# Optimization experiments

Hardware: AMD Instinct MI355X
Metric: run time of the kernel (lower is better)

## Reference

```python
import jax, jax.numpy as jnp
import numpy as np

NU, NI, E = 200000, 100000, 500000
D, H, O = 128, 256, 128  # embedding_dim, hidden_dim, output_dim


def _sage(x_src, x_dst, src, dst, n_dst, W_l, b_l, W_r):
    """PyG SAGEConv (mean aggr): lin_l(mean_j x_src[j]) + lin_r(x_dst)."""
    msgs = x_src[src]                                            # [E, d_in]
    summed = jax.ops.segment_sum(msgs, dst, num_segments=n_dst)  # [n_dst, d_in]
    deg = jax.ops.segment_sum(jnp.ones(src.shape, x_src.dtype), dst, num_segments=n_dst)
    mean = summed / jnp.maximum(deg, 1.0)[:, None]
    return mean @ W_l + b_l + x_dst @ W_r


def setup_inputs() -> dict:
    key = jax.random.key(0)
    ks = jax.random.split(key, 18)

    def w(k, i, o):
        return jax.random.normal(k, (i, o), jnp.float32) / np.float32(np.sqrt(i))

    return {
        "x_user": jax.random.normal(ks[0], (NU, D), jnp.float32),
        "x_item": jax.random.normal(ks[1], (NI, D), jnp.float32),
        "edge_src": jax.random.randint(ks[2], (E,), 0, NU, jnp.int32),
        "edge_dst": jax.random.randint(ks[3], (E,), 0, NI, jnp.int32),
        # layer 1 (encoder): D -> H, one SAGEConv per edge type
        "W_l1_ui": w(ks[4], D, H), "W_r1_ui": w(ks[5], D, H), "b_l1_ui": jnp.zeros((H,), jnp.float32),
        "W_l1_iu": w(ks[6], D, H), "W_r1_iu": w(ks[7], D, H), "b_l1_iu": jnp.zeros((H,), jnp.float32),
        # layer 2 (projection): H -> O
        "W_l2_ui": w(ks[8], H, O), "W_r2_ui": w(ks[9], H, O), "b_l2_ui": jnp.zeros((O,), jnp.float32),
        "W_l2_iu": w(ks[10], H, O), "W_r2_iu": w(ks[11], H, O), "b_l2_iu": jnp.zeros((O,), jnp.float32),
    }


def reference(x_user, x_item, edge_src, edge_dst,
              W_l1_ui, W_r1_ui, b_l1_ui, W_l1_iu, W_r1_iu, b_l1_iu,
              W_l2_ui, W_r2_ui, b_l2_ui, W_l2_iu, W_r2_iu, b_l2_iu):
    # encoder layer: relu(SAGEConv) per destination node type (dropout=eval/no-op)
    h_item = jax.nn.relu(_sage(x_user, x_item, edge_src, edge_dst, NI, W_l1_ui, b_l1_ui, W_r1_ui))
    h_user = jax.nn.relu(_sage(x_item, x_user, edge_dst, edge_src, NU, W_l1_iu, b_l1_iu, W_r1_iu))
    # extra relu in RecommendationGNN.forward is a no-op after relu
    # projection layer: relu(SAGEConv), dropout=0
    o_item = jax.nn.relu(_sage(h_user, h_item, edge_src, edge_dst, NI, W_l2_ui, b_l2_ui, W_r2_ui))
    o_user = jax.nn.relu(_sage(h_item, h_user, edge_dst, edge_src, NU, W_l2_iu, b_l2_iu, W_r2_iu))
    return (o_user, o_item)
```

## Files before the change

kernel.cpp:

```cpp
#include <hip/hip_runtime.h>
#include <stdint.h>

typedef __attribute__((ext_vector_type(8))) short short8;
typedef __attribute__((ext_vector_type(4))) float f32x4;

#define SCAN_TILE 4096

__device__ __forceinline__ float bf2f(unsigned short u) {
  union { unsigned int i; float f; } v;
  v.i = ((unsigned int)u) << 16;
  return v.f;
}
__device__ __forceinline__ unsigned short f2bf(float f) {
  union { float f; unsigned int i; } v;
  v.f = f;
  unsigned int u = v.i;
  return (unsigned short)((u + 0x7FFFu + ((u >> 16) & 1u)) >> 16);
}
__device__ __forceinline__ unsigned int pack2(float a, float b) {
  return (unsigned int)f2bf(a) | ((unsigned int)f2bf(b) << 16);
}
__device__ __forceinline__ void add2(float& a, float& b, unsigned int v) {
  a += bf2f((unsigned short)(v & 0xffff));
  b += bf2f((unsigned short)(v >> 16));
}

__device__ __forceinline__ size_t fragS(int row, int k) {
  return ((size_t)(row >> 4) * 8 + (size_t)(k >> 5)) * 512
       + (size_t)((((row & 15) + (((k >> 3) & 3) << 4)) << 3) + (k & 7));
}

__global__ __launch_bounds__(256) void build_wt_all(
    const float* __restrict__ Wl1ui, const float* __restrict__ Wr1ui,
    const float* __restrict__ Wl1iu, const float* __restrict__ Wr1iu,
    const float* __restrict__ Wl2ui, const float* __restrict__ Wr2ui,
    const float* __restrict__ Wl2iu, const float* __restrict__ Wr2iu,
    unsigned short* __restrict__ WT1ui, unsigned short* __restrict__ WT1iu,
    unsigned short* __restrict__ WT2lui, unsigned short* __restrict__ WT2rui,
    unsigned short* __restrict__ WT2liu, unsigned short* __restrict__ WT2riu)
{
  int idx = blockIdx.x * 256 + threadIdx.x;
  const float *W1, *W2 = nullptr;
  unsigned short* WT;
  int K1, N, rel;
  if (idx < 65536)       { W1 = Wl1ui; W2 = Wr1ui; WT = WT1ui;  K1 = 128; N = 256; rel = idx; }
  else if (idx < 131072) { W1 = Wl1iu; W2 = Wr1iu; WT = WT1iu;  K1 = 128; N = 256; rel = idx - 65536; }
  else if (idx < 163840) { W1 = Wl2ui;             WT = WT2lui; K1 = 256; N = 128; rel = idx - 131072; }
  else if (idx < 196608) { W1 = Wr2ui;             WT = WT2rui; K1 = 256; N = 128; rel = idx - 163840; }
  else if (idx < 229376) { W1 = Wl2iu;             WT = WT2liu; K1 = 256; N = 128; rel = idx - 196608; }
  else                   { W1 = Wr2iu;             WT = WT2riu; K1 = 256; N = 128; rel = idx - 229376; }
  int n = rel >> 8;
  int k = rel & 255;
  float v = (k < K1) ? W1[(size_t)k * N + n] : W2[(size_t)(k - K1) * N + n];
  WT[fragS(n, k)] = f2bf(v);
}

__global__ __launch_bounds__(256) void hist(
    const int* __restrict__ esrc, const int* __restrict__ edst,
    int* __restrict__ cntAll, int NI, int E)
{
  int e = blockIdx.x * 256 + threadIdx.x;
  if (e >= E) return;
  atomicAdd(&cntAll[edst[e]], 1);
  atomicAdd(&cntAll[NI + esrc[e]], 1);
}

__global__ __launch_bounds__(256) void scan_p1(
    const int* __restrict__ cnt, int* __restrict__ tileSums, int NA)
{
  __shared__ int red[256];
  int b = blockIdx.x, t = threadIdx.x;
  int base = b * SCAN_TILE;
  int s = 0;
  for (int i = t; i < SCAN_TILE; i += 256) {
    int g = base + i;
    if (g < NA) s += cnt[g];
  }
  red[t] = s;
  __syncthreads();
  for (int d = 128; d > 0; d >>= 1) {
    if (t < d) red[t] += red[t + d];
    __syncthreads();
  }
  if (t == 0) tileSums[b] = red[0];
}

__global__ __launch_bounds__(256) void scan_p2(
    int* __restrict__ tileSums, int nTiles, int* __restrict__ offEnd)
{
  __shared__ int buf[256];
  int t = threadIdx.x;
  int v = (t < nTiles) ? tileSums[t] : 0;
  buf[t] = v;
  __syncthreads();
  for (int d = 1; d < 256; d <<= 1) {
    int x = (t >= d) ? buf[t - d] : 0;
    __syncthreads();
    buf[t] += x;
    __syncthreads();
  }
  if (t < nTiles) tileSums[t] = buf[t] - v;
  if (t == nTiles - 1) *offEnd = buf[t];
}

__global__ __launch_bounds__(256) void scan_p3(
    const int* __restrict__ cnt, const int* __restrict__ tileSums,
    int* __restrict__ off, int NA)
{
  __shared__ int red[256];
  int b = blockIdx.x, t = threadIdx.x;
  int base = b * SCAN_TILE + t * 16;
  int loc[16];
  int s = 0;
#pragma unroll
  for (int i = 0; i < 16; ++i) {
    int g = base + i;
    loc[i] = (g < NA) ? cnt[g] : 0;
    s += loc[i];
  }
  red[t] = s;
  __syncthreads();
  for (int d = 1; d < 256; d <<= 1) {
    int x = (t >= d) ? red[t - d] : 0;
    __syncthreads();
    red[t] += x;
    __syncthreads();
  }
  int run = tileSums[b] + red[t] - s;
#pragma unroll
  for (int i = 0; i < 16; ++i) {
    int g = base + i;
    if (g < NA) off[g] = run;
    run += loc[i];
  }
}

__global__ __launch_bounds__(256) void fill_idx(
    const int* __restrict__ esrc, const int* __restrict__ edst,
    const int* __restrict__ offAll, int* __restrict__ curAll,
    int* __restrict__ idxAll, int NI, int E)
{
  int e = blockIdx.x * 256 + threadIdx.x;
  if (e >= E) return;
  int s = esrc[e], d = edst[e];
  int pI = offAll[d] + atomicAdd(&curAll[d], 1);
  idxAll[pI] = s;
  int pU = offAll[NI + s] + atomicAdd(&curAll[NI + s], 1);
  idxAll[pU] = d;
}

__global__ __launch_bounds__(256) void build_acat(
    const float* __restrict__ xu, const float* __restrict__ xi,
    const int* __restrict__ idxAll, const int* __restrict__ offAll,
    unsigned short* __restrict__ AcatI, unsigned short* __restrict__ AcatU,
    int NI, int NA)
{
  int w = (blockIdx.x * 256 + threadIdx.x) >> 6;
  if (w >= NA) return;
  int l = threadIdx.x & 63;
  int h = l >> 5;
  int lh = l & 31;
  bool isItem = (w < NI);
  const float* xo = isItem ? xu : xi;
  const float* xs = isItem ? xi : xu;
  unsigned short* Acat = isItem ? AcatI : AcatU;
  int n = isItem ? w : (w - NI);
  int s = offAll[w], e = offAll[w + 1];

  f32x4 xv = (f32x4){0.f, 0.f, 0.f, 0.f};
  if (h) xv = *(const f32x4*)(xs + (size_t)n * 128 + lh * 4);

  f32x4 acc = (f32x4){0.f, 0.f, 0.f, 0.f};
  int j = s + h;
  for (; j + 2 < e; j += 4) {
    int g0 = idxAll[j];
    int g1 = idxAll[j + 2];
    f32x4 v0 = *(const f32x4*)(xo + (size_t)g0 * 128 + lh * 4);
    f32x4 v1 = *(const f32x4*)(xo + (size_t)g1 * 128 + lh * 4);
    acc += v0 + v1;
  }
  if (j < e) {
    int g = idxAll[j];
    acc += *(const f32x4*)(xo + (size_t)g * 128 + lh * 4);
  }

#pragma unroll
  for (int c = 0; c < 4; ++c)
    acc[c] += __shfl_xor(acc[c], 32, 64);

  float inv = 1.0f / (float)max(e - s, 1);
  int kb = (h ? 128 : 0) + lh * 4;
  float x0, x1, x2, x3;
  if (h) { x0 = xv[0]; x1 = xv[1]; x2 = xv[2]; x3 = xv[3]; }
  else   { x0 = acc[0] * inv; x1 = acc[1] * inv; x2 = acc[2] * inv; x3 = acc[3] * inv; }
  uint2 o;
  o.x = pack2(x0, x1);
  o.y = pack2(x2, x3);
  *(uint2*)(Acat + fragS(n, kb)) = o;
}

__global__ __launch_bounds__(256) void seg_mean(
    const unsigned int* __restrict__ pU, const unsigned int* __restrict__ pI,
    const int* __restrict__ idxAll, const int* __restrict__ offAll,
    unsigned int* __restrict__ m2I, unsigned int* __restrict__ m2U,
    int NI, int NA)
{
  int w = (blockIdx.x * 256 + threadIdx.x) >> 6;
  if (w >= NA) return;
  int l = threadIdx.x & 63;
  int q = l >> 4;
  int lq = l & 15;
  bool isItem = (w < NI);
  const unsigned int* p = isItem ? pU : pI;
  unsigned int* m2 = isItem ? m2I : m2U;
  int n = isItem ? w : (w - NI);
  int s = offAll[w], e = offAll[w + 1];

  float a0 = 0.f, a1 = 0.f, a2 = 0.f, a3 = 0.f,
        a4 = 0.f, a5 = 0.f, a6 = 0.f, a7 = 0.f;

  int j = s + q;
  for (; j + 4 < e; j += 8) {
    int g0 = idxAll[j];
    int g1 = idxAll[j + 4];
    uint4 v0 = *(const uint4*)(p + (size_t)g0 * 64 + lq * 4);
    uint4 v1 = *(const uint4*)(p + (size_t)g1 * 64 + lq * 4);
    add2(a0, a1, v0.x); add2(a2, a3, v0.y); add2(a4, a5, v0.z); add2(a6, a7, v0.w);
    add2(a0, a1, v1.x); add2(a2, a3, v1.y); add2(a4, a5, v1.z); add2(a6, a7, v1.w);
  }
  if (j < e) {
    int g = idxAll[j];
    uint4 v = *(const uint4*)(p + (size_t)g * 64 + lq * 4);
    add2(a0, a1, v.x); add2(a2, a3, v.y); add2(a4, a5, v.z); add2(a6, a7, v.w);
  }

  float r[8] = {a0, a1, a2, a3, a4, a5, a6, a7};
#pragma unroll
  for (int c = 0; c < 8; ++c) {
    r[c] += __shfl_xor(r[c], 16, 64);
    r[c] += __shfl_xor(r[c], 32, 64);
  }

  float inv = 1.0f / (float)max(e - s, 1);
  if (q == 0) {
    uint4 o;
    o.x = pack2(r[0] * inv, r[1] * inv);
    o.y = pack2(r[2] * inv, r[3] * inv);
    o.z = pack2(r[4] * inv, r[5] * inv);
    o.w = pack2(r[6] * inv, r[7] * inv);
    *(uint4*)(m2 + (size_t)n * 64 + lq * 4) = o;
  }
}

__global__ __launch_bounds__(256, 3) void gemm_flat(
    const unsigned short* __restrict__ Afrag,
    const unsigned short* __restrict__ Bfrag,
    const float* __restrict__ bias,
    const unsigned short* __restrict__ Madd,
    void* __restrict__ outp,
    int outF32, int outFrag, int M, int N, int doRelu)
{
  const int lane = threadIdx.x & 63;
  const int wave = threadIdx.x >> 6;
  const int m0 = blockIdx.x * 128 + (wave >> 1) * 64;
  const int n0 = blockIdx.y * 128 + (wave & 1) * 64;
  const int r16 = lane & 15;
  const int quad = lane >> 4;

  const uint4* A = (const uint4*)Afrag;
  const uint4* B = (const uint4*)Bfrag;
  const size_t aB = (size_t)(m0 >> 4) * 512 + lane;
  const size_t bB = (size_t)(n0 >> 4) * 512 + lane;

  f32x4 acc[4][4];
#pragma unroll
  for (int i = 0; i < 4; ++i)
#pragma unroll
    for (int j = 0; j < 4; ++j) acc[i][j] = (f32x4){0.f, 0.f, 0.f, 0.f};

#pragma unroll
  for (int k0 = 0; k0 < 8; ++k0) {
    short8 av[4], bv[4];
#pragma unroll
    for (int g = 0; g < 4; ++g) {
      uint4 ta = A[aB + (size_t)(g * 8 + k0) * 64];
      uint4 tb = B[bB + (size_t)(g * 8 + k0) * 64];
      av[g] = *(const short8*)&ta;
      bv[g] = *(const short8*)&tb;
    }
#pragma unroll
    for (int mg = 0; mg < 4; ++mg)
#pragma unroll
      for (int ng = 0; ng < 4; ++ng)
        acc[mg][ng] = __builtin_amdgcn_mfma_f32_16x16x32_bf16(bv[ng], av[mg], acc[mg][ng], 0, 0, 0);
  }

#pragma unroll
  for (int mg = 0; mg < 4; ++mg) {
    int row = m0 + mg * 16 + r16;
    if (row < M) {
#pragma unroll
      for (int ng = 0; ng < 4; ++ng) {
        int col = n0 + ng * 16 + quad * 4;
        f32x4 v = acc[mg][ng];
        if (bias) {
          f32x4 b4 = *(const f32x4*)(bias + col);
          v += b4;
        }
        if (Madd) {
          uint2 md = *(const uint2*)(Madd + (size_t)row * 128 + col);
          v[0] += bf2f((unsigned short)(md.x & 0xffff));
          v[1] += bf2f((unsigned short)(md.x >> 16));
          v[2] += bf2f((unsigned short)(md.y & 0xffff));
          v[3] += bf2f((unsigned short)(md.y >> 16));
        }
        if (doRelu) {
          v[0] = fmaxf(v[0], 0.0f); v[1] = fmaxf(v[1], 0.0f);
          v[2] = fmaxf(v[2], 0.0f); v[3] = fmaxf(v[3], 0.0f);
        }
        if (outF32) {
          *(f32x4*)((float*)outp + (size_t)row * N + col) = v;
        } else {
          uint2 o;
          o.x = pack2(v[0], v[1]);
          o.y = pack2(v[2], v[3]);
          if (outFrag) *(uint2*)((unsigned short*)outp + fragS(row, col)) = o;
          else         *(uint2*)((unsigned short*)outp + (size_t)row * N + col) = o;
        }
      }
    }
  }
}

extern "C" void kernel_launch(void* const* d_in, const int* in_sizes, int n_in,
                              void* d_out, int out_size, void* d_ws, size_t ws_size,
                              hipStream_t stream)
{
  const float* x_user  = (const float*)d_in[0];
  const float* x_item  = (const float*)d_in[1];
  const int*   esrc    = (const int*)d_in[2];
  const int*   edst    = (const int*)d_in[3];
  const float* W_l1_ui = (const float*)d_in[4];
  const float* W_r1_ui = (const float*)d_in[5];
  const float* b_l1_ui = (const float*)d_in[6];
  const float* W_l1_iu = (const float*)d_in[7];
  const float* W_r1_iu = (const float*)d_in[8];
  const float* b_l1_iu = (const float*)d_in[9];
  const float* W_l2_ui = (const float*)d_in[10];
  const float* W_r2_ui = (const float*)d_in[11];
  const float* b_l2_ui = (const float*)d_in[12];
  const float* W_l2_iu = (const float*)d_in[13];
  const float* W_r2_iu = (const float*)d_in[14];
  const float* b_l2_iu = (const float*)d_in[15];

  const int NU = in_sizes[0] / 128;
  const int NI = in_sizes[1] / 128;
  const int E  = in_sizes[2];
  const int NA = NI + NU;
  const int MI = ((NI + 127) / 128) * 128;
  const int MU = ((NU + 127) / 128) * 128;

  char* ws = (char*)d_ws;
  size_t off = 0;
  auto alloc = [&](size_t bytes) -> void* {
    void* p = ws + off;
    off += (bytes + 255) & ~(size_t)255;
    return p;
  };

  int* cntAll = (int*)alloc((size_t)NA * 4);
  int* curAll = (int*)alloc((size_t)NA * 4);
  size_t zeroBytes = off;
  int* offAll   = (int*)alloc((size_t)(NA + 1) * 4);
  int* tileSums = (int*)alloc(256 * 4);
  int* idxAll   = (int*)alloc((size_t)2 * E * 4);
  unsigned short* WT1_ui  = (unsigned short*)alloc(256 * 256 * 2);
  unsigned short* WT1_iu  = (unsigned short*)alloc(256 * 256 * 2);
  unsigned short* WT2l_ui = (unsigned short*)alloc(128 * 256 * 2);
  unsigned short* WT2r_ui = (unsigned short*)alloc(128 * 256 * 2);
  unsigned short* WT2l_iu = (unsigned short*)alloc(128 * 256 * 2);
  unsigned short* WT2r_iu = (unsigned short*)alloc(128 * 256 * 2);
  unsigned short* h_item = (unsigned short*)alloc((size_t)MI * 256 * 2);
  unsigned short* h_user = (unsigned short*)alloc((size_t)MU * 256 * 2);
  char* R = (char*)alloc((size_t)(MI + MU) * 256 * 2);
  unsigned short* Acat_item = (unsigned short*)R;
  unsigned short* Acat_user = (unsigned short*)(R + (size_t)MI * 256 * 2);
  unsigned short* p_user = (unsigned short*)R;
  unsigned short* p_item = (unsigned short*)(R + (size_t)NU * 128 * 2);
  unsigned short* m2I    = (unsigned short*)(R + (size_t)(NU + NI) * 128 * 2);
  unsigned short* m2U    = (unsigned short*)(R + (size_t)(NU + 2 * NI) * 128 * 2);

  float* out = (float*)d_out;

  hipMemsetAsync(ws, 0, zeroBytes, stream);

  build_wt_all<<<1024, 256, 0, stream>>>(
      W_l1_ui, W_r1_ui, W_l1_iu, W_r1_iu, W_l2_ui, W_r2_ui, W_l2_iu, W_r2_iu,
      WT1_ui, WT1_iu, WT2l_ui, WT2r_ui, WT2l_iu, WT2r_iu);

  int egrid = (E + 255) / 256;
  int nTiles = (NA + SCAN_TILE - 1) / SCAN_TILE;
  hist<<<egrid, 256, 0, stream>>>(esrc, edst, cntAll, NI, E);
  scan_p1<<<nTiles, 256, 0, stream>>>(cntAll, tileSums, NA);
  scan_p2<<<1, 256, 0, stream>>>(tileSums, nTiles, offAll + NA);
  scan_p3<<<nTiles, 256, 0, stream>>>(cntAll, tileSums, offAll, NA);
  fill_idx<<<egrid, 256, 0, stream>>>(esrc, edst, offAll, curAll, idxAll, NI, E);

  build_acat<<<(NA * 64 + 255) / 256, 256, 0, stream>>>(
      x_user, x_item, idxAll, offAll, Acat_item, Acat_user, NI, NA);

  dim3 gI(MI / 128, 2), gU(MU / 128, 2);
  gemm_flat<<<gI, 256, 0, stream>>>(Acat_item, WT1_ui, b_l1_ui, nullptr,
                                    h_item, 0, 1, NI, 256, 1);
  gemm_flat<<<gU, 256, 0, stream>>>(Acat_user, WT1_iu, b_l1_iu, nullptr,
                                    h_user, 0, 1, NU, 256, 1);

  dim3 pGu(MU / 128, 1), pGi(MI / 128, 1);
  gemm_flat<<<pGu, 256, 0, stream>>>(h_user, WT2l_ui, nullptr, nullptr,
                                     p_user, 0, 0, NU, 128, 0);
  gemm_flat<<<pGi, 256, 0, stream>>>(h_item, WT2l_iu, nullptr, nullptr,
                                     p_item, 0, 0, NI, 128, 0);

  seg_mean<<<(NA * 64 + 255) / 256, 256, 0, stream>>>(
      (const unsigned int*)p_user, (const unsigned int*)p_item,
      idxAll, offAll, (unsigned int*)m2I, (unsigned int*)m2U, NI, NA);

  gemm_flat<<<pGi, 256, 0, stream>>>(h_item, WT2r_ui, b_l2_ui, m2I,
                                     out + (size_t)NU * 128, 1, 0, NI, 128, 1);
  gemm_flat<<<pGu, 256, 0, stream>>>(h_user, WT2r_iu, b_l2_iu, m2U,
                                     out, 1, 0, NU, 128, 1);
}
```

Measured before the change: 1.000 ms.

## Split K-concatenated operands into separate lo/hi fragment buffers and repack gathers

The single K=256 fragment layout is replaced by two K=128 halves, so the GEMM reads the mean and self features from separate buffers. The self features are converted to bf16 fragments by a standalone conv_x kernel instead of inside the gather. The gather kernels now map several nodes per wave, two per wave in build_mean and four in seg_mean, which removes the cross-lane shuffle reductions. This cuts wasted lanes for low-degree nodes, at the cost of less memory parallelism per node, an extra launch, and an extra pass over x.

```diff
diff --git a/kernel.cpp b/kernel.cpp
--- a/kernel.cpp
+++ b/kernel.cpp
@@ -25,8 +25,8 @@
   b += bf2f((unsigned short)(v >> 16));
 }
 
-__device__ __forceinline__ size_t fragS(int row, int k) {
-  return ((size_t)(row >> 4) * 8 + (size_t)(k >> 5)) * 512
+__device__ __forceinline__ size_t fragS128(int row, int k) {
+  return ((size_t)(row >> 4) * 4 + (size_t)(k >> 5)) * 512
        + (size_t)((((row & 15) + (((k >> 3) & 3) << 4)) << 3) + (k & 7));
 }
 
@@ -35,24 +35,56 @@
     const float* __restrict__ Wl1iu, const float* __restrict__ Wr1iu,
     const float* __restrict__ Wl2ui, const float* __restrict__ Wr2ui,
     const float* __restrict__ Wl2iu, const float* __restrict__ Wr2iu,
-    unsigned short* __restrict__ WT1ui, unsigned short* __restrict__ WT1iu,
-    unsigned short* __restrict__ WT2lui, unsigned short* __restrict__ WT2rui,
-    unsigned short* __restrict__ WT2liu, unsigned short* __restrict__ WT2riu)
+    unsigned short* __restrict__ T1ui_l, unsigned short* __restrict__ T1ui_h,
+    unsigned short* __restrict__ T1iu_l, unsigned short* __restrict__ T1iu_h,
+    unsigned short* __restrict__ T2lui_l, unsigned short* __restrict__ T2lui_h,
+    unsigned short* __restrict__ T2rui_l, unsigned short* __restrict__ T2rui_h,
+    unsigned short* __restrict__ T2liu_l, unsigned short* __restrict__ T2liu_h,
+    unsigned short* __restrict__ T2riu_l, unsigned short* __restrict__ T2riu_h)
 {
   int idx = blockIdx.x * 256 + threadIdx.x;
-  const float *W1, *W2 = nullptr;
-  unsigned short* WT;
-  int K1, N, rel;
-  if (idx < 65536)       { W1 = Wl1ui; W2 = Wr1ui; WT = WT1ui;  K1 = 128; N = 256; rel = idx; }
-  else if (idx < 131072) { W1 = Wl1iu; W2 = Wr1iu; WT = WT1iu;  K1 = 128; N = 256; rel = idx - 65536; }
-  else if (idx < 163840) { W1 = Wl2ui;             WT = WT2lui; K1 = 256; N = 128; rel = idx - 131072; }
-  else if (idx < 196608) { W1 = Wr2ui;             WT = WT2rui; K1 = 256; N = 128; rel = idx - 163840; }
-  else if (idx < 229376) { W1 = Wl2iu;             WT = WT2liu; K1 = 256; N = 128; rel = idx - 196608; }
-  else                   { W1 = Wr2iu;             WT = WT2riu; K1 = 256; N = 128; rel = idx - 229376; }
+  const float *W1, *W2;
+  unsigned short *lo, *hi;
+  int N, rel;
+  if (idx < 65536)       { W1 = Wl1ui; W2 = Wr1ui;          lo = T1ui_l;  hi = T1ui_h;  N = 256; rel = idx; }
+  else if (idx < 131072) { W1 = Wl1iu; W2 = Wr1iu;          lo = T1iu_l;  hi = T1iu_h;  N = 256; rel = idx - 65536; }
+  else if (idx < 163840) { W1 = Wl2ui; W2 = Wl2ui + 128*128; lo = T2lui_l; hi = T2lui_h; N = 128; rel = idx - 131072; }
+  else if (idx < 196608) { W1 = Wr2ui; W2 = Wr2ui + 128*128; lo = T2rui_l; hi = T2rui_h; N = 128; rel = idx - 163840; }
+  else if (idx < 229376) { W1 = Wl2iu; W2 = Wl2iu + 128*128; lo = T2liu_l; hi = T2liu_h; N = 128; rel = idx - 196608; }
+  else                   { W1 = Wr2iu; W2 = Wr2iu + 128*128; lo = T2riu_l; hi = T2riu_h; N = 128; rel = idx - 229376; }
   int n = rel >> 8;
   int k = rel & 255;
-  float v = (k < K1) ? W1[(size_t)k * N + n] : W2[(size_t)(k - K1) * N + n];
-  WT[fragS(n, k)] = f2bf(v);
+  float v = (k < 128) ? W1[(size_t)k * N + n] : W2[(size_t)(k - 128) * N + n];
+  if (k < 128) lo[fragS128(n, k)] = f2bf(v);
+  else         hi[fragS128(n, k - 128)] = f2bf(v);
+}
+
+__global__ __launch_bounds__(256) void conv_x(
+    const float* __restrict__ xu, const float* __restrict__ xi,
+    uint4* __restrict__ XfI, uint4* __restrict__ XfU,
+    int NI, int NU, int MI, int MU)
+{
+  int u = blockIdx.x * 256 + threadIdx.x;
+  int unitsI = MI * 16;
+  const float* x; uint4* Xf; int M; int rel;
+  if (u < unitsI) { x = xi; Xf = XfI; M = NI; rel = u; }
+  else {
+    rel = u - unitsI;
+    if (rel >= MU * 16) return;
+    x = xu; Xf = XfU; M = NU;
+  }
+  int c = rel >> 6;
+  int s = rel & 63;
+  int row = ((c >> 2) << 4) + (s & 15);
+  int k = ((c & 3) << 5) + ((s >> 4) << 3);
+  uint4 o = make_uint4(0u, 0u, 0u, 0u);
+  if (row < M) {
+    f32x4 a = *(const f32x4*)(x + (size_t)row * 128 + k);
+    f32x4 b = *(const f32x4*)(x + (size_t)row * 128 + k + 4);
+    o.x = pack2(a[0], a[1]); o.y = pack2(a[2], a[3]);
+    o.z = pack2(b[0], b[1]); o.w = pack2(b[2], b[3]);
+  }
+  Xf[rel] = o;
 }
 
 __global__ __launch_bounds__(256) void hist(
@@ -149,32 +181,29 @@
   idxAll[pU] = d;
 }
 
-__global__ __launch_bounds__(256) void build_acat(
+__global__ __launch_bounds__(256) void build_mean(
     const float* __restrict__ xu, const float* __restrict__ xi,
     const int* __restrict__ idxAll, const int* __restrict__ offAll,
-    unsigned short* __restrict__ AcatI, unsigned short* __restrict__ AcatU,
+    unsigned short* __restrict__ MfI, unsigned short* __restrict__ MfU,
     int NI, int NA)
 {
-  int w = (blockIdx.x * 256 + threadIdx.x) >> 6;
-  if (w >= NA) return;
+  int w2 = (blockIdx.x * 256 + threadIdx.x) >> 6;
   int l = threadIdx.x & 63;
   int h = l >> 5;
   int lh = l & 31;
-  bool isItem = (w < NI);
+  int node = w2 * 2 + h;
+  if (node >= NA) return;
+  bool isItem = (node < NI);
   const float* xo = isItem ? xu : xi;
-  const float* xs = isItem ? xi : xu;
-  unsigned short* Acat = isItem ? AcatI : AcatU;
-  int n = isItem ? w : (w - NI);
-  int s = offAll[w], e = offAll[w + 1];
-
-  f32x4 xv = (f32x4){0.f, 0.f, 0.f, 0.f};
-  if (h) xv = *(const f32x4*)(xs + (size_t)n * 128 + lh * 4);
+  unsigned short* Mf = isItem ? MfI : MfU;
+  int n = isItem ? node : (node - NI);
+  int s = offAll[node], e = offAll[node + 1];
 
   f32x4 acc = (f32x4){0.f, 0.f, 0.f, 0.f};
-  int j = s + h;
-  for (; j + 2 < e; j += 4) {
+  int j = s;
+  for (; j + 1 < e; j += 2) {
     int g0 = idxAll[j];
-    int g1 = idxAll[j + 2];
+    int g1 = idxAll[j + 1];
     f32x4 v0 = *(const f32x4*)(xo + (size_t)g0 * 128 + lh * 4);
     f32x4 v1 = *(const f32x4*)(xo + (size_t)g1 * 128 + lh * 4);
     acc += v0 + v1;
@@ -184,19 +213,11 @@
     acc += *(const f32x4*)(xo + (size_t)g * 128 + lh * 4);
   }
 
-#pragma unroll
-  for (int c = 0; c < 4; ++c)
-    acc[c] += __shfl_xor(acc[c], 32, 64);
-
   float inv = 1.0f / (float)max(e - s, 1);
-  int kb = (h ? 128 : 0) + lh * 4;
-  float x0, x1, x2, x3;
-  if (h) { x0 = xv[0]; x1 = xv[1]; x2 = xv[2]; x3 = xv[3]; }
-  else   { x0 = acc[0] * inv; x1 = acc[1] * inv; x2 = acc[2] * inv; x3 = acc[3] * inv; }
   uint2 o;
-  o.x = pack2(x0, x1);
-  o.y = pack2(x2, x3);
-  *(uint2*)(Acat + fragS(n, kb)) = o;
+  o.x = pack2(acc[0] * inv, acc[1] * inv);
+  o.y = pack2(acc[2] * inv, acc[3] * inv);
+  *(uint2*)(Mf + fragS128(n, lh * 4)) = o;
 }
 
 __global__ __launch_bounds__(256) void seg_mean(
@@ -205,24 +226,25 @@
     unsigned int* __restrict__ m2I, unsigned int* __restrict__ m2U,
     int NI, int NA)
 {
-  int w = (blockIdx.x * 256 + threadIdx.x) >> 6;
-  if (w >= NA) return;
+  int w4 = (blockIdx.x * 256 + threadIdx.x) >> 6;
   int l = threadIdx.x & 63;
   int q = l >> 4;
   int lq = l & 15;
-  bool isItem = (w < NI);
+  int node = w4 * 4 + q;
+  if (node >= NA) return;
+  bool isItem = (node < NI);
   const unsigned int* p = isItem ? pU : pI;
   unsigned int* m2 = isItem ? m2I : m2U;
-  int n = isItem ? w : (w - NI);
-  int s = offAll[w], e = offAll[w + 1];
+  int n = isItem ? node : (node - NI);
+  int s = offAll[node], e = offAll[node + 1];
 
   float a0 = 0.f, a1 = 0.f, a2 = 0.f, a3 = 0.f,
         a4 = 0.f, a5 = 0.f, a6 = 0.f, a7 = 0.f;
 
-  int j = s + q;
-  for (; j + 4 < e; j += 8) {
+  int j = s;
+  for (; j + 1 < e; j += 2) {
     int g0 = idxAll[j];
-    int g1 = idxAll[j + 4];
+    int g1 = idxAll[j + 1];
     uint4 v0 = *(const uint4*)(p + (size_t)g0 * 64 + lq * 4);
     uint4 v1 = *(const uint4*)(p + (size_t)g1 * 64 + lq * 4);
     add2(a0, a1, v0.x); add2(a2, a3, v0.y); add2(a4, a5, v0.z); add2(a6, a7, v0.w);
@@ -234,30 +256,21 @@
     add2(a0, a1, v.x); add2(a2, a3, v.y); add2(a4, a5, v.z); add2(a6, a7, v.w);
   }
 
-  float r[8] = {a0, a1, a2, a3, a4, a5, a6, a7};
-#pragma unroll
-  for (int c = 0; c < 8; ++c) {
-    r[c] += __shfl_xor(r[c], 16, 64);
-    r[c] += __shfl_xor(r[c], 32, 64);
-  }
-
   float inv = 1.0f / (float)max(e - s, 1);
-  if (q == 0) {
-    uint4 o;
-    o.x = pack2(r[0] * inv, r[1] * inv);
-    o.y = pack2(r[2] * inv, r[3] * inv);
-    o.z = pack2(r[4] * inv, r[5] * inv);
-    o.w = pack2(r[6] * inv, r[7] * inv);
-    *(uint4*)(m2 + (size_t)n * 64 + lq * 4) = o;
-  }
+  uint4 o;
+  o.x = pack2(a0 * inv, a1 * inv);
+  o.y = pack2(a2 * inv, a3 * inv);
+  o.z = pack2(a4 * inv, a5 * inv);
+  o.w = pack2(a6 * inv, a7 * inv);
+  *(uint4*)(m2 + (size_t)n * 64 + lq * 4) = o;
 }
 
 __global__ __launch_bounds__(256, 3) void gemm_flat(
-    const unsigned short* __restrict__ Afrag,
-    const unsigned short* __restrict__ Bfrag,
+    const unsigned short* __restrict__ Alo, const unsigned short* __restrict__ Ahi,
+    const unsigned short* __restrict__ Blo, const unsigned short* __restrict__ Bhi,
     const float* __restrict__ bias,
     const unsigned short* __restrict__ Madd,
-    void* __restrict__ outp,
+    void* __restrict__ outp, unsigned short* __restrict__ outHi,
     int outF32, int outFrag, int M, int N, int doRelu)
 {
   const int lane = threadIdx.x & 63;
@@ -267,10 +280,12 @@
   const int r16 = lane & 15;
   const int quad = lane >> 4;
 
-  const uint4* A = (const uint4*)Afrag;
-  const uint4* B = (const uint4*)Bfrag;
-  const size_t aB = (size_t)(m0 >> 4) * 512 + lane;
-  const size_t bB = (size_t)(n0 >> 4) * 512 + lane;
+  const uint4* AL = (const uint4*)Alo;
+  const uint4* AH = (const uint4*)Ahi;
+  const uint4* BL = (const uint4*)Blo;
+  const uint4* BH = (const uint4*)Bhi;
+  const size_t aB = (size_t)(m0 >> 4) * 256 + lane;
+  const size_t bB = (size_t)(n0 >> 4) * 256 + lane;
 
   f32x4 acc[4][4];
 #pragma unroll
@@ -279,12 +294,28 @@
     for (int j = 0; j < 4; ++j) acc[i][j] = (f32x4){0.f, 0.f, 0.f, 0.f};
 
 #pragma unroll
-  for (int k0 = 0; k0 < 8; ++k0) {
+  for (int k0 = 0; k0 < 4; ++k0) {
     short8 av[4], bv[4];
 #pragma unroll
     for (int g = 0; g < 4; ++g) {
-      uint4 ta = A[aB + (size_t)(g * 8 + k0) * 64];
-      uint4 tb = B[bB + (size_t)(g * 8 + k0) * 64];
+      uint4 ta = AL[aB + (size_t)(g * 4 + k0) * 64];
+      uint4 tb = BL[bB + (size_t)(g * 4 + k0) * 64];
+      av[g] = *(const short8*)&ta;
+      bv[g] = *(const short8*)&tb;
+    }
+#pragma unroll
+    for (int mg = 0; mg < 4; ++mg)
+#pragma unroll
+      for (int ng = 0; ng < 4; ++ng)
+        acc[mg][ng] = __builtin_amdgcn_mfma_f32_16x16x32_bf16(bv[ng], av[mg], acc[mg][ng], 0, 0, 0);
+  }
+#pragma unroll
+  for (int k0 = 0; k0 < 4; ++k0) {
+    short8 av[4], bv[4];
+#pragma unroll
+    for (int g = 0; g < 4; ++g) {
+      uint4 ta = AH[aB + (size_t)(g * 4 + k0) * 64];
+      uint4 tb = BH[bB + (size_t)(g * 4 + k0) * 64];
       av[g] = *(const short8*)&ta;
       bv[g] = *(const short8*)&tb;
     }
@@ -324,8 +355,12 @@
           uint2 o;
           o.x = pack2(v[0], v[1]);
           o.y = pack2(v[2], v[3]);
-          if (outFrag) *(uint2*)((unsigned short*)outp + fragS(row, col)) = o;
-          else         *(uint2*)((unsigned short*)outp + (size_t)row * N + col) = o;
+          if (outFrag) {
+            if (col < 128) *(uint2*)((unsigned short*)outp + fragS128(row, col)) = o;
+            else           *(uint2*)(outHi + fragS128(row, col - 128)) = o;
+          } else {
+            *(uint2*)((unsigned short*)outp + (size_t)row * N + col) = o;
+          }
         }
       }
     }
@@ -374,17 +409,27 @@
   int* offAll   = (int*)alloc((size_t)(NA + 1) * 4);
   int* tileSums = (int*)alloc(256 * 4);
   int* idxAll   = (int*)alloc((size_t)2 * E * 4);
-  unsigned short* WT1_ui  = (unsigned short*)alloc(256 * 256 * 2);
-  unsigned short* WT1_iu  = (unsigned short*)alloc(256 * 256 * 2);
-  unsigned short* WT2l_ui = (unsigned short*)alloc(128 * 256 * 2);
-  unsigned short* WT2r_ui = (unsigned short*)alloc(128 * 256 * 2);
-  unsigned short* WT2l_iu = (unsigned short*)alloc(128 * 256 * 2);
-  unsigned short* WT2r_iu = (unsigned short*)alloc(128 * 256 * 2);
+  unsigned short* T1ui_l  = (unsigned short*)alloc(256 * 128 * 2);
+  unsigned short* T1ui_h  = (unsigned short*)alloc(256 * 128 * 2);
+  unsigned short* T1iu_l  = (unsigned short*)alloc(256 * 128 * 2);
+  unsigned short* T1iu_h  = (unsigned short*)alloc(256 * 128 * 2);
+  unsigned short* T2lui_l = (unsigned short*)alloc(128 * 128 * 2);
+  unsigned short* T2lui_h = (unsigned short*)alloc(128 * 128 * 2);
+  unsigned short* T2rui_l = (unsigned short*)alloc(128 * 128 * 2);
+  unsigned short* T2rui_h = (unsigned short*)alloc(128 * 128 * 2);
+  unsigned short* T2liu_l = (unsigned short*)alloc(128 * 128 * 2);
+  unsigned short* T2liu_h = (unsigned short*)alloc(128 * 128 * 2);
+  unsigned short* T2riu_l = (unsigned short*)alloc(128 * 128 * 2);
+  unsigned short* T2riu_h = (unsigned short*)alloc(128 * 128 * 2);
   unsigned short* h_item = (unsigned short*)alloc((size_t)MI * 256 * 2);
+  unsigned short* h_item_hi = h_item + (size_t)MI * 128;
   unsigned short* h_user = (unsigned short*)alloc((size_t)MU * 256 * 2);
+  unsigned short* h_user_hi = h_user + (size_t)MU * 128;
   char* R = (char*)alloc((size_t)(MI + MU) * 256 * 2);
-  unsigned short* Acat_item = (unsigned short*)R;
-  unsigned short* Acat_user = (unsigned short*)(R + (size_t)MI * 256 * 2);
+  unsigned short* Mf_item = (unsigned short*)R;
+  unsigned short* Mf_user = (unsigned short*)(R + (size_t)MI * 128 * 2);
+  unsigned short* Xf_item = (unsigned short*)(R + (size_t)(MI + MU) * 128 * 2);
+  unsigned short* Xf_user = (unsigned short*)(R + (size_t)(2 * MI + MU) * 128 * 2);
   unsigned short* p_user = (unsigned short*)R;
   unsigned short* p_item = (unsigned short*)(R + (size_t)NU * 128 * 2);
   unsigned short* m2I    = (unsigned short*)(R + (size_t)(NU + NI) * 128 * 2);
@@ -396,7 +441,12 @@
 
   build_wt_all<<<1024, 256, 0, stream>>>(
       W_l1_ui, W_r1_ui, W_l1_iu, W_r1_iu, W_l2_ui, W_r2_ui, W_l2_iu, W_r2_iu,
-      WT1_ui, WT1_iu, WT2l_ui, WT2r_ui, WT2l_iu, WT2r_iu);
+      T1ui_l, T1ui_h, T1iu_l, T1iu_h,
+      T2lui_l, T2lui_h, T2rui_l, T2rui_h, T2liu_l, T2liu_h, T2riu_l, T2riu_h);
+
+  int units = (MI + MU) * 16;
+  conv_x<<<(units + 255) / 256, 256, 0, stream>>>(
+      x_user, x_item, (uint4*)Xf_item, (uint4*)Xf_user, NI, NU, MI, MU);
 
   int egrid = (E + 255) / 256;
   int nTiles = (NA + SCAN_TILE - 1) / SCAN_TILE;
@@ -406,27 +456,29 @@
   scan_p3<<<nTiles, 256, 0, stream>>>(cntAll, tileSums, offAll, NA);
   fill_idx<<<egrid, 256, 0, stream>>>(esrc, edst, offAll, curAll, idxAll, NI, E);
 
-  build_acat<<<(NA * 64 + 255) / 256, 256, 0, stream>>>(
-      x_user, x_item, idxAll, offAll, Acat_item, Acat_user, NI, NA);
+  int waves1 = (NA + 1) / 2;
+  build_mean<<<(waves1 * 64 + 255) / 256, 256, 0, stream>>>(
+      x_user, x_item, idxAll, offAll, Mf_item, Mf_user, NI, NA);
 
   dim3 gI(MI / 128, 2), gU(MU / 128, 2);
-  gemm_flat<<<gI, 256, 0, stream>>>(Acat_item, WT1_ui, b_l1_ui, nullptr,
-                                    h_item, 0, 1, NI, 256, 1);
-  gemm_flat<<<gU, 256, 0, stream>>>(Acat_user, WT1_iu, b_l1_iu, nullptr,
-                                    h_user, 0, 1, NU, 256, 1);
+  gemm_flat<<<gI, 256, 0, stream>>>(Mf_item, Xf_item, T1ui_l, T1ui_h, b_l1_ui,
+                                    nullptr, h_item, h_item_hi, 0, 1, NI, 256, 1);
+  gemm_flat<<<gU, 256, 0, stream>>>(Mf_user, Xf_user, T1iu_l, T1iu_h, b_l1_iu,
+                                    nullptr, h_user, h_user_hi, 0, 1, NU, 256, 1);
 
   dim3 pGu(MU / 128, 1), pGi(MI / 128, 1);
-  gemm_flat<<<pGu, 256, 0, stream>>>(h_user, WT2l_ui, nullptr, nullptr,
-                                     p_user, 0, 0, NU, 128, 0);
-  gemm_flat<<<pGi, 256, 0, stream>>>(h_item, WT2l_iu, nullptr, nullptr,
-                                     p_item, 0, 0, NI, 128, 0);
-
-  seg_mean<<<(NA * 64 + 255) / 256, 256, 0, stream>>>(
+  gemm_flat<<<pGu, 256, 0, stream>>>(h_user, h_user_hi, T2lui_l, T2lui_h, nullptr,
+                                     nullptr, p_user, nullptr, 0, 0, NU, 128, 0);
+  gemm_flat<<<pGi, 256, 0, stream>>>(h_item, h_item_hi, T2liu_l, T2liu_h, nullptr,
+                                     nullptr, p_item, nullptr, 0, 0, NI, 128, 0);
+
+  int waves2 = (NA + 3) / 4;
+  seg_mean<<<(waves2 * 64 + 255) / 256, 256, 0, stream>>>(
       (const unsigned int*)p_user, (const unsigned int*)p_item,
       idxAll, offAll, (unsigned int*)m2I, (unsigned int*)m2U, NI, NA);
 
-  gemm_flat<<<pGi, 256, 0, stream>>>(h_item, WT2r_ui, b_l2_ui, m2I,
-                                     out + (size_t)NU * 128, 1, 0, NI, 128, 1);
-  gemm_flat<<<pGu, 256, 0, stream>>>(h_user, WT2r_iu, b_l2_iu, m2U,
-                                     out, 1, 0, NU, 128, 1);
-}
+  gemm_flat<<<pGi, 256, 0, stream>>>(h_item, h_item_hi, T2rui_l, T2rui_h, b_l2_ui,
+                                     m2I, out + (size_t)NU * 128, nullptr, 1, 0, NI, 128, 1);
+  gemm_flat<<<pGu, 256, 0, stream>>>(h_user, h_user_hi, T2riu_l, T2riu_h, b_l2_iu,
+                                     m2U, out, nullptr, 1, 0, NU, 128, 1);
+}
```

Measured after the change: 854.5 us. 14.6% less time.
